# Kernel tuning notes

Hardware: AMD Instinct MI355X
Metric: run time of the kernel (lower is better)

The kernel has to match this reference:

```python
import jax, jax.numpy as jnp
import numpy as np

TS, BS, N, F = 4, 16, 2048, 64
ALPHA = 0.2      # LeakyReLU negative slope
NEG = -9e15      # mask value from original code


def setup_inputs() -> dict:
    key = jax.random.key(0)
    k0, k1, k2, k3 = jax.random.split(key, 4)
    x = jax.random.normal(k0, (TS, BS * N, 1), dtype=jnp.float32)
    # sparse-ish symmetric-ish adjacency with self loops (only >0 test matters)
    adj = (jax.random.uniform(k1, (N, N)) < 0.05).astype(jnp.float32)
    adj = jnp.maximum(adj, jnp.eye(N, dtype=jnp.float32))
    W = jax.random.normal(k2, (TS, 1, F), dtype=jnp.float32) * 0.1
    a = jax.random.normal(k3, (TS, 2 * F, 1), dtype=jnp.float32) * 0.1
    return {"x": x, "adj": adj, "W": W, "a": a, "bs": BS}


def _gat_layer(x_t, adj, W_t, a_t, bs):
    # x_t: (bs*N, 1) -> h: (bs, N, F)
    n = x_t.shape[0] // bs
    f = W_t.shape[-1]
    h = x_t.reshape(bs, n, 1) @ W_t
    # e_ij = leakyrelu([h_i || h_j] @ a) = leakyrelu(h_i@a1 + h_j@a2)
    a1, a2 = a_t[:f, 0], a_t[f:, 0]
    s1 = h @ a1            # (bs, N)
    s2 = h @ a2            # (bs, N)
    e = jax.nn.leaky_relu(s1[:, :, None] + s2[:, None, :], ALPHA)  # (bs, N, N)
    att = jnp.where(adj[None] > 0, e, NEG)
    # dropout is a no-op in eval mode; then extra positivity mask from original
    att = jnp.where(att > 0, att, NEG)
    att = jax.nn.softmax(att, axis=2)
    h_prime = att @ h      # (bs, N, F)
    return jax.nn.elu(h_prime)


def reference(x, adj, W, a, bs):
    ts = x.shape[0]
    outs = []
    for t in range(ts):  # small fixed layer count, distinct params per layer
        out = _gat_layer(x[t], adj, W[t], a[t], bs)
        outs.append(out[:, -1, :])  # target-region node is last
    return jnp.stack(outs, 1)  # (bs, ts, F)
```

## Files before the change

### kernel.cpp

```cpp
#include <hip/hip_runtime.h>
#include <math.h>

#define TS 4
#define BS 16
#define NN 2048
#define FF 64
#define NEGV -9.0e15f

__global__ __launch_bounds__(256) void gat_last_row_kernel(
    const float* __restrict__ x,
    const float* __restrict__ adj,
    const float* __restrict__ W,
    const float* __restrict__ a,
    float* __restrict__ out)
{
    const int blk = blockIdx.x;
    const int t   = blk >> 4;
    const int b   = blk & 15;
    const int tid = threadIdx.x;

    const float* Wt = W + t * FF;
    const float* at = a + t * 2 * FF;
    float A1 = 0.f, A2 = 0.f;
#pragma unroll
    for (int f = 0; f < FF; ++f) {
        float w = Wt[f];
        A1 += w * at[f];
        A2 += w * at[FF + f];
    }

    const float* xb = x + (size_t)t * (BS * NN) + (size_t)b * NN;
    const float  x_last = xb[NN - 1];
    const float  s1 = x_last * A1;
    const float* adjrow = adj + (size_t)(NN - 1) * NN;

    float m = -INFINITY, l = 0.f, y = 0.f;

    const float4* x4 = (const float4*)xb;
    const float4* a4 = (const float4*)adjrow;
#pragma unroll
    for (int k = tid; k < NN / 4; k += 256) {
        float4 xv = x4[k];
        float4 av = a4[k];
#pragma unroll
        for (int u = 0; u < 4; ++u) {
            float xj   = (&xv.x)[u];
            float adjv = (&av.x)[u];
            float s    = s1 + xj * A2;
            float att  = (adjv > 0.f && s > 0.f) ? s : NEGV;
            float mn   = fmaxf(m, att);
            float sa   = expf(m - mn);
            float pe   = expf(att - mn);
            l = l * sa + pe;
            y = y * sa + pe * xj;
            m = mn;
        }
    }

#pragma unroll
    for (int off = 32; off; off >>= 1) {
        float m2 = __shfl_xor(m, off);
        float l2 = __shfl_xor(l, off);
        float y2 = __shfl_xor(y, off);
        float mn = fmaxf(m, m2);
        float sa = expf(m - mn);
        float sb = expf(m2 - mn);
        l = l * sa + l2 * sb;
        y = y * sa + y2 * sb;
        m = mn;
    }

    __shared__ float sm[4], sl[4], sy[4];
    __shared__ float yfinal;
    const int wave = tid >> 6;
    const int lane = tid & 63;
    if (lane == 0) { sm[wave] = m; sl[wave] = l; sy[wave] = y; }
    __syncthreads();
    if (tid == 0) {
        float M = sm[0], L = sl[0], Y = sy[0];
#pragma unroll
        for (int wv = 1; wv < 4; ++wv) {
            float mn = fmaxf(M, sm[wv]);
            float sa = expf(M - mn);
            float sb = expf(sm[wv] - mn);
            L = L * sa + sl[wv] * sb;
            Y = Y * sa + sy[wv] * sb;
            M = mn;
        }
        yfinal = Y / L;
    }
    __syncthreads();

    if (tid < FF) {
        float v = yfinal * Wt[tid];
        out[(size_t)b * (TS * FF) + t * FF + tid] = (v > 0.f) ? v : expm1f(v);
    }
}

extern "C" void kernel_launch(void* const* d_in, const int* in_sizes, int n_in,
                              void* d_out, int out_size, void* d_ws, size_t ws_size,
                              hipStream_t stream) {
    const float* x   = (const float*)d_in[0];
    const float* adj = (const float*)d_in[1];
    const float* W   = (const float*)d_in[2];
    const float* a   = (const float*)d_in[3];

    float* out = (float*)d_out;

    gat_last_row_kernel<<<TS * BS, 256, 0, stream>>>(x, adj, W, a, out);
}
```

Measured before the change: 74.26 us.

## Replace online softmax with two-pass block max then exp-sum reduction

Each thread now loads its 8 elements into registers up front, computes the attention logits, and finds a block-wide max with wave shuffles and shared memory. It then does a single exp per element and sums with plain additive reductions, instead of running an online-softmax recurrence with two exps per element and rescaling during every merge. The A1/A2 dot products are computed in parallel across lanes with shuffles rather than by a serial 64-iteration loop in every thread. The kernel is small and latency-bound, so the gain comes from a shorter dependent chain, at the cost of an extra block barrier.

```diff
diff --git a/kernel.cpp b/kernel.cpp
--- a/kernel.cpp
+++ b/kernel.cpp
@@ -14,85 +14,75 @@
     const float* __restrict__ a,
     float* __restrict__ out)
 {
-    const int blk = blockIdx.x;
-    const int t   = blk >> 4;
-    const int b   = blk & 15;
-    const int tid = threadIdx.x;
+    const int blk  = blockIdx.x;
+    const int t    = blk >> 4;
+    const int b    = blk & 15;
+    const int tid  = threadIdx.x;
+    const int lane = tid & 63;
+    const int wave = tid >> 6;
 
     const float* Wt = W + t * FF;
     const float* at = a + t * 2 * FF;
-    float A1 = 0.f, A2 = 0.f;
+    const float w   = Wt[lane];
+    float pa1 = w * at[lane];
+    float pa2 = w * at[FF + lane];
 #pragma unroll
-    for (int f = 0; f < FF; ++f) {
-        float w = Wt[f];
-        A1 += w * at[f];
-        A2 += w * at[FF + f];
+    for (int off = 32; off; off >>= 1) {
+        pa1 += __shfl_xor(pa1, off);
+        pa2 += __shfl_xor(pa2, off);
     }
+    const float A1 = pa1, A2 = pa2;
 
     const float* xb = x + (size_t)t * (BS * NN) + (size_t)b * NN;
-    const float  x_last = xb[NN - 1];
-    const float  s1 = x_last * A1;
+    const float  s1 = xb[NN - 1] * A1;
     const float* adjrow = adj + (size_t)(NN - 1) * NN;
-
-    float m = -INFINITY, l = 0.f, y = 0.f;
 
     const float4* x4 = (const float4*)xb;
     const float4* a4 = (const float4*)adjrow;
+    float4 xv0 = x4[tid], xv1 = x4[tid + 256];
+    float4 av0 = a4[tid], av1 = a4[tid + 256];
+
+    float xs[8]  = { xv0.x, xv0.y, xv0.z, xv0.w, xv1.x, xv1.y, xv1.z, xv1.w };
+    float as[8]  = { av0.x, av0.y, av0.z, av0.w, av1.x, av1.y, av1.z, av1.w };
+    float att[8];
 #pragma unroll
-    for (int k = tid; k < NN / 4; k += 256) {
-        float4 xv = x4[k];
-        float4 av = a4[k];
-#pragma unroll
-        for (int u = 0; u < 4; ++u) {
-            float xj   = (&xv.x)[u];
-            float adjv = (&av.x)[u];
-            float s    = s1 + xj * A2;
-            float att  = (adjv > 0.f && s > 0.f) ? s : NEGV;
-            float mn   = fmaxf(m, att);
-            float sa   = expf(m - mn);
-            float pe   = expf(att - mn);
-            l = l * sa + pe;
-            y = y * sa + pe * xj;
-            m = mn;
-        }
+    for (int u = 0; u < 8; ++u) {
+        float s = fmaf(xs[u], A2, s1);
+        att[u] = (as[u] > 0.f && s > 0.f) ? s : NEGV;
     }
 
+    float mloc = fmaxf(fmaxf(fmaxf(att[0], att[1]), fmaxf(att[2], att[3])),
+                       fmaxf(fmaxf(att[4], att[5]), fmaxf(att[6], att[7])));
+#pragma unroll
+    for (int off = 32; off; off >>= 1)
+        mloc = fmaxf(mloc, __shfl_xor(mloc, off));
+
+    __shared__ float smax[4];
+    if (lane == 0) smax[wave] = mloc;
+    __syncthreads();
+    const float M = fmaxf(fmaxf(smax[0], smax[1]), fmaxf(smax[2], smax[3]));
+
+    float l = 0.f, y = 0.f;
+#pragma unroll
+    for (int u = 0; u < 8; ++u) {
+        float p = expf(att[u] - M);
+        l += p;
+        y  = fmaf(p, xs[u], y);
+    }
 #pragma unroll
     for (int off = 32; off; off >>= 1) {
-        float m2 = __shfl_xor(m, off);
-        float l2 = __shfl_xor(l, off);
-        float y2 = __shfl_xor(y, off);
-        float mn = fmaxf(m, m2);
-        float sa = expf(m - mn);
-        float sb = expf(m2 - mn);
-        l = l * sa + l2 * sb;
-        y = y * sa + y2 * sb;
-        m = mn;
+        l += __shfl_xor(l, off);
+        y += __shfl_xor(y, off);
     }
 
-    __shared__ float sm[4], sl[4], sy[4];
-    __shared__ float yfinal;
-    const int wave = tid >> 6;
-    const int lane = tid & 63;
-    if (lane == 0) { sm[wave] = m; sl[wave] = l; sy[wave] = y; }
-    __syncthreads();
-    if (tid == 0) {
-        float M = sm[0], L = sl[0], Y = sy[0];
-#pragma unroll
-        for (int wv = 1; wv < 4; ++wv) {
-            float mn = fmaxf(M, sm[wv]);
-            float sa = expf(M - mn);
-            float sb = expf(sm[wv] - mn);
-            L = L * sa + sl[wv] * sb;
-            Y = Y * sa + sy[wv] * sb;
-            M = mn;
-        }
-        yfinal = Y / L;
-    }
+    __shared__ float sl[4], sy[4];
+    if (lane == 0) { sl[wave] = l; sy[wave] = y; }
     __syncthreads();
 
     if (tid < FF) {
-        float v = yfinal * Wt[tid];
+        float L  = (sl[0] + sl[1]) + (sl[2] + sl[3]);
+        float Y  = (sy[0] + sy[1]) + (sy[2] + sy[3]);
+        float v  = (Y / L) * w;
         out[(size_t)b * (TS * FF) + t * FF + tid] = (v > 0.f) ? v : expm1f(v);
     }
 }
```

Result: faster. 71.24 us (-4.1%).
